# Kernel optimization log

Measured on AMD Instinct MI355X. Metric: run time of the kernel, lower is better.

Reference implementation:

```python
import jax, jax.numpy as jnp
import numpy as np

B, S, E = 4, 2048, 768
DFF = 4 * E
EPS = 1e-5


def _layernorm(x, g, b):
    mu = jnp.mean(x, axis=-1, keepdims=True)
    var = jnp.mean(jnp.square(x - mu), axis=-1, keepdims=True)
    return (x - mu) * jax.lax.rsqrt(var + EPS) * g + b


def setup_inputs() -> dict:
    key = jax.random.key(0)
    ks = jax.random.split(key, 16)
    w = lambda k, shp: jax.random.normal(k, shp, dtype=jnp.float32) * 0.02
    inp = {
        "x": jax.random.normal(ks[0], (B, S, E), dtype=jnp.float32),
        "kv": jax.random.normal(ks[1], (B, S, E), dtype=jnp.float32),
        "wq_w": w(ks[2], (E, E)), "wq_b": jnp.zeros((E,), jnp.float32),
        "wk_w": w(ks[3], (E, E)), "wk_b": jnp.zeros((E,), jnp.float32),
        "wv_w": w(ks[4], (E, E)), "wv_b": jnp.zeros((E,), jnp.float32),
        "ln1_g": jnp.ones((E,), jnp.float32), "ln1_b": jnp.zeros((E,), jnp.float32),
        "wq2_w": w(ks[5], (E, E)), "wq2_b": jnp.zeros((E,), jnp.float32),
        "wk2_w": w(ks[6], (E, E)), "wk2_b": jnp.zeros((E,), jnp.float32),
        "wv2_w": w(ks[7], (E, E)), "wv2_b": jnp.zeros((E,), jnp.float32),
        "ln2_g": jnp.ones((E,), jnp.float32), "ln2_b": jnp.zeros((E,), jnp.float32),
        "w1": w(ks[8], (DFF, E)), "b1": jnp.zeros((DFF,), jnp.float32),
        "w2": w(ks[9], (E, DFF)), "b2": jnp.zeros((E,), jnp.float32),
        "ln3_g": jnp.ones((E,), jnp.float32), "ln3_b": jnp.zeros((E,), jnp.float32),
    }
    return inp


def reference(x, kv, wq_w, wq_b, wk_w, wk_b, wv_w, wv_b, ln1_g, ln1_b,
              wq2_w, wq2_b, wk2_w, wk2_b, wv2_w, wv2_b, ln2_g, ln2_b,
              w1, b1, w2, b2, ln3_g, ln3_b):
    scalar = 1.0 / np.sqrt(E).astype(np.float32)
    mask_value = jnp.finfo(x.dtype).min
    s = x.shape[1]
    causal = jnp.triu(jnp.ones((s, s), dtype=bool), k=1)  # True above diagonal -> masked

    # ---- causal self-attention (single head, full E) ----
    q = x @ wq_w.T + wq_b
    k = x @ wk_w.T + wk_b
    v = x @ wv_w.T + wv_b
    scores = jnp.einsum('bqe,bke->bqk', q, k) * scalar
    scores = jnp.where(causal, mask_value, scores)
    h1 = jnp.einsum('bqk,bke->bqe', jax.nn.softmax(scores, axis=-1), v)
    x = _layernorm(x + h1, ln1_g, ln1_b)

    # ---- cross-attention over kv (no mask) ----
    q2 = x @ wq2_w.T + wq2_b
    k2 = kv @ wk2_w.T + wk2_b
    v2 = kv @ wv2_w.T + wv2_b
    scores2 = jnp.einsum('bqe,bke->bqk', q2, k2) * scalar
    h2 = jnp.einsum('bqk,bke->bqe', jax.nn.softmax(scores2, axis=-1), v2)
    x = _layernorm(x + h2, ln2_g, ln2_b)

    # ---- MLP: Linear -> ReLU -> Linear -> ReLU (note trailing ReLU) ----
    h = jax.nn.relu(x @ w1.T + b1)
    mlp = jax.nn.relu(h @ w2.T + b2)
    return _layernorm(x + mlp, ln3_g, ln3_b)
```

## Files before the change

### kernel.cpp

```cpp
#include <hip/hip_runtime.h>
#include <hip/hip_bf16.h>
#include <math.h>


typedef __bf16 bf16_t;
typedef bf16_t bf16x4 __attribute__((ext_vector_type(4)));
typedef bf16_t bf16x8 __attribute__((ext_vector_type(8)));
typedef float f32x4 __attribute__((ext_vector_type(4)));

struct MMDesc {
    const bf16_t* A;
    const bf16_t* B;
    const float* bias;
    __hip_bfloat16* C;
    float* lsum;
    int koff;
    int trans;
};
struct MMArgs { MMDesc g[8]; };

__device__ __forceinline__ int xcd_swz(int bid, int nwg) {
    const int q = nwg >> 3, r = nwg & 7;
    const int xcd = bid & 7, o = bid >> 3;
    const int base = (xcd < r) ? xcd * (q + 1) : r * (q + 1) + (xcd - r) * q;
    return base + o;
}

__device__ __forceinline__ void load16(const bf16_t* g, bf16_t* l) {
    __builtin_amdgcn_global_load_lds(
        (const __attribute__((address_space(1))) unsigned int*)g,
        (__attribute__((address_space(3))) unsigned int*)l, 16, 0, 0);
}

__device__ __forceinline__ void rd4(const bf16_t* p, int s0, int s1, bf16x8 f[4][2]) {
#pragma unroll
    for (int i = 0; i < 4; ++i) {
        f[i][0] = *(const bf16x8*)(p + i * 1024 + s0);
        f[i][1] = *(const bf16x8*)(p + i * 1024 + s1);
    }
}
__device__ __forceinline__ void rd2(const bf16_t* p, int s0, int s1, bf16x8 f[2][2]) {
#pragma unroll
    for (int i = 0; i < 2; ++i) {
        f[i][0] = *(const bf16x8*)(p + i * 1024 + s0);
        f[i][1] = *(const bf16x8*)(p + i * 1024 + s1);
    }
}

#define SBAR asm volatile("s_barrier" ::: "memory")
#define SCH  __builtin_amdgcn_sched_barrier(0)
#define PBAR do { SCH; SBAR; SCH; } while (0)
#define PRIO1 __builtin_amdgcn_s_setprio(1)
#define PRIO0 __builtin_amdgcn_s_setprio(0)
#define VMC6 asm volatile("s_waitcnt vmcnt(6)" ::: "memory")

#define QMFMA(mh, nh, BF) do { \
    _Pragma("unroll") \
    for (int ks = 0; ks < 2; ++ks) \
    _Pragma("unroll") \
    for (int mi = 0; mi < 4; ++mi) \
    _Pragma("unroll") \
    for (int ni = 0; ni < 2; ++ni) \
        acc[(mh) * 4 + mi][(nh) * 2 + ni] = __builtin_amdgcn_mfma_f32_16x16x32_bf16( \
            af[mi][ks], BF[ni][ks], acc[(mh) * 4 + mi][(nh) * 2 + ni], 0, 0, 0); \
} while (0)

__device__ __forceinline__ void mm8_core(
    const bf16_t* Ag, const bf16_t* Bg, int lda, int ldb, int K,
    bf16_t* lds, int w, int l, f32x4 acc[8][4])
{
    const long ldal = lda, ldbl = ldb;
    const int fr = l & 15, kq = l >> 4;
    const int rr = w * 8 + (l >> 3);
    const int c8e = ((l & 7) ^ (l >> 3)) * 8;
    const bf16_t* As = Ag + (long)rr * ldal + c8e;
    const bf16_t* Bs = Bg + (long)rr * ldbl + c8e;
    const int s0 = ((0 + kq) ^ (fr & 7)) * 8;
    const int s1 = ((4 + kq) ^ (fr & 7)) * 8;
    const bf16_t* lA = lds + ((w >> 2) * 64 + fr) * 64;
    const bf16_t* lB = lds + 16384 + ((w & 3) * 32 + fr) * 64;
    bf16_t* stA = lds + w * 512;
    bf16_t* stB = lds + 16384 + w * 512;

    auto stg = [&](int b, int isB, int h, int t) {
        const long ld = isB ? ldbl : ldal;
        const bf16_t* g = (isB ? Bs : As) + (long)h * 128 * ld + (long)t * 64;
        bf16_t* d = (isB ? stB : stA) + b * 32768 + h * 8192;
        load16(g, d);
        load16(g + 64 * ld, d + 4096);
    };

    bf16x8 af[4][2], bf0[2][2], bf1[2][2];
    const int NT = K >> 6, NI = NT >> 1;

    stg(0, 0, 0, 0); stg(0, 1, 0, 0); stg(0, 1, 1, 0); stg(0, 0, 1, 0);
    stg(1, 0, 0, 1); stg(1, 1, 0, 1); stg(1, 1, 1, 1);
    VMC6;
    SBAR; SCH;

    for (int i = 0; i < NI; ++i) {
        const int t1 = 2 * i + 1;
        int t2 = 2 * i + 2; if (t2 >= NT) t2 -= 2;
        int t3 = 2 * i + 3; if (t3 >= NT) t3 -= 2;
        rd4(lA, s0, s1, af); rd2(lB, s0, s1, bf0);
        stg(1, 0, 1, t1);
        PBAR; PRIO1; QMFMA(0, 0, bf0); PRIO0;
        rd2(lB + 8192, s0, s1, bf1);
        PBAR; PRIO1; QMFMA(0, 1, bf1); PRIO0;
        rd4(lA + 8192, s0, s1, af);
        stg(0, 0, 0, t2); stg(0, 1, 0, t2);
        PBAR; PRIO1; QMFMA(1, 0, bf0); PRIO0;
        stg(0, 1, 1, t2);
        VMC6;
        PBAR; PRIO1; QMFMA(1, 1, bf1); PRIO0;
        rd4(lA + 32768, s0, s1, af); rd2(lB + 32768, s0, s1, bf0);
        stg(0, 0, 1, t2);
        PBAR; PRIO1; QMFMA(0, 0, bf0); PRIO0;
        rd2(lB + 32768 + 8192, s0, s1, bf1);
        PBAR; PRIO1; QMFMA(0, 1, bf1); PRIO0;
        rd4(lA + 32768 + 8192, s0, s1, af);
        stg(1, 0, 0, t3); stg(1, 1, 0, t3);
        PBAR; PRIO1; QMFMA(1, 0, bf0); PRIO0;
        stg(1, 1, 1, t3);
        VMC6;
        PBAR; PRIO1; QMFMA(1, 1, bf1); PRIO0;
    }
    asm volatile("s_waitcnt vmcnt(0)" ::: "memory");
    SBAR; SCH;
}

template <bool RELU, bool CLAMPK>
__global__ __launch_bounds__(512, 2) void mm8_std(
    MMArgs args, int M, int N, int K, int lda, int ldb, float scale, int GX)
{
    __shared__ __align__(16) bf16_t lds[65536];
    const MMDesc dsc = args.g[blockIdx.z];

    const int lin = xcd_swz(blockIdx.x, gridDim.x);
    const int panel = lin / (8 * GX);
    const int rem = lin - panel * 8 * GX;
    const int bx = rem >> 3;
    const int by = panel * 8 + (rem & 7);
    const int m0 = by * 256, n0 = bx * 256;
    const int tid = threadIdx.x, w = tid >> 6, l = tid & 63;

    f32x4 acc[8][4];
    const f32x4 z4 = {0.f, 0.f, 0.f, 0.f};
#pragma unroll
    for (int i = 0; i < 8; ++i)
#pragma unroll
        for (int j = 0; j < 4; ++j) acc[i][j] = z4;

    int Keff = K;
    if (CLAMPK) {
        int km = (by + 1) * 256 - dsc.koff;
        Keff = km < K ? km : K;
    }
    if (!CLAMPK || Keff > 0)
        mm8_core(dsc.A + (long)m0 * lda, dsc.B + (long)n0 * ldb,
                 lda, ldb, Keff, lds, w, l, acc);

    const int fr = l & 15, erow = (l >> 4) * 4;
    const int wrow = (w >> 2) * 64, wcol = (w & 3) * 32;
    bf16_t* ctb = lds;
    __hip_bfloat16* ct = (__hip_bfloat16*)lds;
#pragma unroll
    for (int mh = 0; mh < 2; ++mh) {
        if (mh) __syncthreads();
#pragma unroll
        for (int nh = 0; nh < 2; ++nh)
#pragma unroll
            for (int ni = 0; ni < 2; ++ni) {
                const int cl = nh * 128 + wcol + ni * 16 + fr;
                const float bv = dsc.bias ? dsc.bias[n0 + cl] : 0.f;
#pragma unroll
                for (int mi = 0; mi < 4; ++mi) {
                    const int lr = wrow + mi * 16 + erow;
                    const f32x4 a = acc[mh * 4 + mi][nh * 2 + ni];
                    if (dsc.trans) {
                        bf16x4 p;
#pragma unroll
                        for (int r = 0; r < 4; ++r) {
                            float v = a[r] * scale + bv;
                            if (RELU) v = fmaxf(v, 0.f);
                            p[r] = (bf16_t)v;
                        }
                        *(bf16x4*)(ctb + cl * 140 + lr) = p;
                    } else {
#pragma unroll
                        for (int r = 0; r < 4; ++r) {
                            float v = a[r] * scale + bv;
                            if (RELU) v = fmaxf(v, 0.f);
                            ct[(lr + r) * 264 + cl] = __float2bfloat16(v);
                        }
                    }
                }
            }
        __syncthreads();
        if (dsc.trans) {
            __hip_bfloat16* base = dsc.C + ((long)(m0 >> 11) * N + n0) * 2048
                                 + (m0 & 2047) + mh * 128;
#pragma unroll
            for (int u = 0; u < 8; ++u) {
                const int e = u * 4096 + tid * 8;
                const int rl = e >> 7, cl = e & 127;
                const bf16_t* src = ctb + rl * 140 + cl;
                const uint2 lo = *(const uint2*)(src);
                const uint2 hi = *(const uint2*)(src + 4);
                const uint4 v = {lo.x, lo.y, hi.x, hi.y};
                *(uint4*)(base + (long)rl * 2048 + cl) = v;
            }
        } else {
            __hip_bfloat16* base = dsc.C + (long)(m0 + mh * 128) * N + n0;
#pragma unroll
            for (int u = 0; u < 8; ++u) {
                const int e = u * 4096 + tid * 8;
                *(uint4*)(base + (long)(e >> 8) * N + (e & 255))
                    = *(const uint4*)(ct + (e >> 8) * 264 + (e & 255));
            }
        }
    }
}

template <bool CAUSAL>
__global__ __launch_bounds__(512, 2) void mm8_exp(
    MMArgs args, int N, int K, int lda, int ldb, float scale, int GX)
{
    __shared__ __align__(16) bf16_t lds[65536];
    const MMDesc dsc = args.g[blockIdx.z];

    int bx, by;
    if (CAUSAL) {
        const int t = xcd_swz(blockIdx.x, gridDim.x);
        by = (int)((sqrtf(8.f * t + 1.f) - 1.f) * 0.5f);
        while ((by + 1) * (by + 2) / 2 <= t) ++by;
        while (by * (by + 1) / 2 > t) --by;
        bx = t - by * (by + 1) / 2;
    } else {
        const int lin = xcd_swz(blockIdx.x, gridDim.x);
        const int panel = lin / (8 * GX);
        const int rem = lin - panel * 8 * GX;
        bx = rem >> 3;
        by = panel * 8 + (rem & 7);
    }
    const int m0 = by * 256, n0 = bx * 256;
    const int tid = threadIdx.x, w = tid >> 6, l = tid & 63;

    f32x4 acc[8][4];
    const f32x4 z4 = {0.f, 0.f, 0.f, 0.f};
#pragma unroll
    for (int i = 0; i < 8; ++i)
#pragma unroll
        for (int j = 0; j < 4; ++j) acc[i][j] = z4;

    mm8_core(dsc.A + (long)m0 * lda, dsc.B + (long)n0 * ldb,
             lda, ldb, K, lds, w, l, acc);

    const int fr = l & 15, erow = (l >> 4) * 4;
    const int wrow = (w >> 2) * 64, wcol = (w & 3) * 32;
    __hip_bfloat16* ct = (__hip_bfloat16*)lds;
#pragma unroll
    for (int mh = 0; mh < 2; ++mh) {
        if (mh) __syncthreads();
#pragma unroll
        for (int mi = 0; mi < 4; ++mi) {
            const int lr = wrow + mi * 16 + erow;
#pragma unroll
            for (int r = 0; r < 4; ++r) {
                const int grow = m0 + mh * 128 + lr + r;
                float rs = 0.f;
#pragma unroll
                for (int nh = 0; nh < 2; ++nh)
#pragma unroll
                    for (int ni = 0; ni < 2; ++ni) {
                        const int cl = nh * 128 + wcol + ni * 16 + fr;
                        float e;
                        if (CAUSAL && (n0 + cl) > grow)
                            e = 0.f;
                        else
                            e = __expf(acc[mh * 4 + mi][nh * 2 + ni][r] * scale);
                        ct[(lr + r) * 264 + cl] = __float2bfloat16(e);
                        rs += e;
                    }
#pragma unroll
                for (int o = 8; o > 0; o >>= 1) rs += __shfl_down(rs, o, 16);
                if ((l & 15) == 0) atomicAdd(&dsc.lsum[grow], rs);
            }
        }
        __syncthreads();
        __hip_bfloat16* base = dsc.C + (long)(m0 + mh * 128) * N + n0;
#pragma unroll
        for (int u = 0; u < 8; ++u) {
            const int e = u * 4096 + tid * 8;
            *(uint4*)(base + (long)(e >> 8) * N + (e & 255))
                = *(const uint4*)(ct + (e >> 8) * 264 + (e & 255));
        }
    }
}

__device__ __forceinline__ float waveReduceSum(float v) {
#pragma unroll
    for (int o = 32; o > 0; o >>= 1) v += __shfl_down(v, o, 64);
    return v;
}
__device__ __forceinline__ float blockReduceSum(float v, float* s) {
    int lane = threadIdx.x & 63, w = threadIdx.x >> 6;
    v = waveReduceSum(v);
    __syncthreads();
    if (lane == 0) s[w] = v;
    __syncthreads();
    return s[0] + s[1] + s[2] + s[3];
}

template <bool BR, bool XF32>
__global__ __launch_bounds__(256) void ln_kernel(
    const float* __restrict__ xf, const __hip_bfloat16* __restrict__ xh,
    const __hip_bfloat16* __restrict__ h1, const __hip_bfloat16* __restrict__ h2,
    const float* __restrict__ hbias, const float* __restrict__ lsum,
    const float* __restrict__ g, const float* __restrict__ beta,
    float* __restrict__ outf, __hip_bfloat16* __restrict__ outb) {
    __shared__ float red[4];
    const int E = 768;
    const long row = blockIdx.x;
    const float hscale = lsum ? (1.f / lsum[row]) : 1.f;

    float vals[3];
    float sum = 0.f;
#pragma unroll
    for (int i = 0; i < 3; ++i) {
        int c = threadIdx.x + i * 256;
        float t = __bfloat162float(h1[row * E + c]) + __bfloat162float(h2[row * E + c]);
        if (BR) t = fmaxf(t + hbias[c], 0.f);
        else t *= hscale;
        float xv = XF32 ? xf[row * E + c] : __bfloat162float(xh[row * E + c]);
        vals[i] = xv + t;
        sum += vals[i];
    }
    sum = blockReduceSum(sum, red);
    const float mean = sum * (1.f / 768.f);

    float ss = 0.f;
#pragma unroll
    for (int i = 0; i < 3; ++i) {
        float d = vals[i] - mean;
        ss += d * d;
    }
    ss = blockReduceSum(ss, red);
    const float inv = rsqrtf(ss * (1.f / 768.f) + 1e-5f);

#pragma unroll
    for (int i = 0; i < 3; ++i) {
        int c = threadIdx.x + i * 256;
        float v = (vals[i] - mean) * inv * g[c] + beta[c];
        if (outf) outf[row * E + c] = v;
        if (outb) outb[row * E + c] = __float2bfloat16(v);
    }
}

struct CvtPtrs {
    const float* s[10];
    __hip_bfloat16* d[10];
};
__global__ __launch_bounds__(256) void cvt_all(CvtPtrs p) {
    int bid = blockIdx.x, seg, off;
    if (bid < 3456) {
        seg = bid / 576;
        off = (bid % 576) * 1024;
    } else if (bid < 8064) {
        int t = bid - 3456;
        seg = 6 + t / 2304;
        off = (t % 2304) * 1024;
    } else {
        int t = bid - 8064;
        seg = 8 + t / 6144;
        off = (t % 6144) * 1024;
    }
    const float* s = p.s[seg];
    __hip_bfloat16* d = p.d[seg];
    int i = off + threadIdx.x * 4;
    float4 v = *(const float4*)(s + i);
    d[i + 0] = __float2bfloat16(v.x);
    d[i + 1] = __float2bfloat16(v.y);
    d[i + 2] = __float2bfloat16(v.z);
    d[i + 3] = __float2bfloat16(v.w);
}

extern "C" void kernel_launch(void* const* d_in, const int* in_sizes, int n_in,
                              void* d_out, int out_size, void* d_ws, size_t ws_size,
                              hipStream_t stream) {
    const int Bb = 4, S = 2048, E = 768, DFF = 3072;
    const int Nr = Bb * S;

    const float* x    = (const float*)d_in[0];
    const float* kv   = (const float*)d_in[1];
    const float* wq_w = (const float*)d_in[2];
    const float* wq_b = (const float*)d_in[3];
    const float* wk_w = (const float*)d_in[4];
    const float* wk_b = (const float*)d_in[5];
    const float* wv_w = (const float*)d_in[6];
    const float* wv_b = (const float*)d_in[7];
    const float* ln1g = (const float*)d_in[8];
    const float* ln1b = (const float*)d_in[9];
    const float* wq2w = (const float*)d_in[10];
    const float* wq2b = (const float*)d_in[11];
    const float* wk2w = (const float*)d_in[12];
    const float* wk2b = (const float*)d_in[13];
    const float* wv2w = (const float*)d_in[14];
    const float* wv2b = (const float*)d_in[15];
    const float* ln2g = (const float*)d_in[16];
    const float* ln2b = (const float*)d_in[17];
    const float* w1   = (const float*)d_in[18];
    const float* b1   = (const float*)d_in[19];
    const float* w2   = (const float*)d_in[20];
    const float* b2   = (const float*)d_in[21];
    const float* ln3g = (const float*)d_in[22];
    const float* ln3b = (const float*)d_in[23];
    float* out = (float*)d_out;

    char* wsp = (char*)d_ws;
    auto alloc = [&](size_t bytes) {
        char* p = wsp;
        wsp += (bytes + 255) & ~(size_t)255;
        return p;
    };
    const size_t nSE = (size_t)Nr * E;
    const size_t nSS = (size_t)Bb * S * S;
    __hip_bfloat16* Pb   = (__hip_bfloat16*)alloc(nSS * 2);
    __hip_bfloat16* qb   = (__hip_bfloat16*)alloc(nSE * 2);
    __hip_bfloat16* kb   = (__hip_bfloat16*)alloc(nSE * 2);
    __hip_bfloat16* hffb = Pb;
    __hip_bfloat16* vtb  = (__hip_bfloat16*)alloc(nSE * 2);
    __hip_bfloat16* xb   = (__hip_bfloat16*)alloc(nSE * 2);
    __hip_bfloat16* kvb  = (__hip_bfloat16*)alloc(nSE * 2);
    __hip_bfloat16* actb = (__hip_bfloat16*)alloc(nSE * 2);
    __hip_bfloat16* hA   = (__hip_bfloat16*)alloc(nSE * 2);
    __hip_bfloat16* hB   = (__hip_bfloat16*)alloc(nSE * 2);
    __hip_bfloat16* wqb   = (__hip_bfloat16*)alloc((size_t)E * E * 2);
    __hip_bfloat16* wkb   = (__hip_bfloat16*)alloc((size_t)E * E * 2);
    __hip_bfloat16* wvb   = (__hip_bfloat16*)alloc((size_t)E * E * 2);
    __hip_bfloat16* wq2bm = (__hip_bfloat16*)alloc((size_t)E * E * 2);
    __hip_bfloat16* wk2bm = (__hip_bfloat16*)alloc((size_t)E * E * 2);
    __hip_bfloat16* wv2bm = (__hip_bfloat16*)alloc((size_t)E * E * 2);
    __hip_bfloat16* w1b   = (__hip_bfloat16*)alloc((size_t)DFF * E * 2);
    __hip_bfloat16* w2b   = (__hip_bfloat16*)alloc((size_t)E * DFF * 2);
    float* lsum1 = (float*)alloc((size_t)Nr * 4);
    float* lsum2 = (float*)alloc((size_t)Nr * 4);

    __hip_bfloat16* k2b  = (__hip_bfloat16*)d_out;
    __hip_bfloat16* vtb2 = k2b + nSE;

    const float scale = 1.0f / sqrtf((float)E);
    const dim3 blk(256);
    const dim3 blk5(512);

    hipMemsetAsync(lsum1, 0, (size_t)Nr * 4 * 2, stream);

    CvtPtrs cp;
    cp.s[0] = wq_w; cp.d[0] = wqb;
    cp.s[1] = wk_w; cp.d[1] = wkb;
    cp.s[2] = wv_w; cp.d[2] = wvb;
    cp.s[3] = wq2w; cp.d[3] = wq2bm;
    cp.s[4] = wk2w; cp.d[4] = wk2bm;
    cp.s[5] = wv2w; cp.d[5] = wv2bm;
    cp.s[6] = w1;   cp.d[6] = w1b;
    cp.s[7] = w2;   cp.d[7] = w2b;
    cp.s[8] = x;    cp.d[8] = xb;
    cp.s[9] = kv;   cp.d[9] = kvb;
    cvt_all<<<8064 + 12288, blk, 0, stream>>>(cp);

    {
        MMArgs a{};
        a.g[0] = {(const bf16_t*)xb,  (const bf16_t*)wqb,   wq_b, qb,   nullptr, 0, 0};
        a.g[1] = {(const bf16_t*)xb,  (const bf16_t*)wkb,   wk_b, kb,   nullptr, 0, 0};
        a.g[2] = {(const bf16_t*)xb,  (const bf16_t*)wvb,   wv_b, vtb,  nullptr, 0, 1};
        a.g[3] = {(const bf16_t*)kvb, (const bf16_t*)wk2bm, wk2b, k2b,  nullptr, 0, 0};
        a.g[4] = {(const bf16_t*)kvb, (const bf16_t*)wv2bm, wv2b, vtb2, nullptr, 0, 1};
        mm8_std<false, false><<<dim3(96, 1, 5), blk5, 0, stream>>>(
            a, Nr, E, E, E, E, 1.f, 3);
    }
    {
        MMArgs a{};
        for (int b = 0; b < 4; ++b)
            a.g[b] = {(const bf16_t*)qb + (long)b * S * E,
                      (const bf16_t*)kb + (long)b * S * E, nullptr,
                      Pb + (long)b * S * S, lsum1 + b * S, 0, 0};
        mm8_exp<true><<<dim3(36, 1, 4), blk5, 0, stream>>>(a, S, E, E, E, scale, 8);
    }
    {
        MMArgs a{};
        for (int b = 0; b < 4; ++b)
            for (int ks = 0; ks < 2; ++ks)
                a.g[b * 2 + ks] = {(const bf16_t*)Pb + (long)b * S * S + ks * 1024,
                                   (const bf16_t*)vtb + (long)b * E * S + ks * 1024,
                                   nullptr, (ks ? hB : hA) + (long)b * S * E,
                                   nullptr, ks * 1024, 0};
        mm8_std<false, true><<<dim3(24, 1, 8), blk5, 0, stream>>>(
            a, S, E, 1024, S, S, 1.f, 3);
    }
    ln_kernel<false, true><<<Nr, blk, 0, stream>>>(
        x, nullptr, hA, hB, nullptr, lsum1, ln1g, ln1b, nullptr, actb);

    {
        MMArgs a{};
        a.g[0] = {(const bf16_t*)actb, (const bf16_t*)wq2bm, wq2b, qb, nullptr, 0, 0};
        mm8_std<false, false><<<dim3(96, 1, 1), blk5, 0, stream>>>(
            a, Nr, E, E, E, E, 1.f, 3);
    }
    {
        MMArgs a{};
        for (int b = 0; b < 4; ++b)
            a.g[b] = {(const bf16_t*)qb + (long)b * S * E,
                      (const bf16_t*)k2b + (long)b * S * E, nullptr,
                      Pb + (long)b * S * S, lsum2 + b * S, 0, 0};
        mm8_exp<false><<<dim3(64, 1, 4), blk5, 0, stream>>>(a, S, E, E, E, scale, 8);
    }
    {
        MMArgs a{};
        for (int b = 0; b < 4; ++b)
            for (int ks = 0; ks < 2; ++ks)
                a.g[b * 2 + ks] = {(const bf16_t*)Pb + (long)b * S * S + ks * 1024,
                                   (const bf16_t*)vtb2 + (long)b * E * S + ks * 1024,
                                   nullptr, (ks ? hB : hA) + (long)b * S * E,
                                   nullptr, 0, 0};
        mm8_std<false, false><<<dim3(24, 1, 8), blk5, 0, stream>>>(
            a, S, E, 1024, S, S, 1.f, 3);
    }
    ln_kernel<false, false><<<Nr, blk, 0, stream>>>(
        nullptr, actb, hA, hB, nullptr, lsum2, ln2g, ln2b, nullptr, actb);

    {
        MMArgs a{};
        a.g[0] = {(const bf16_t*)actb, (const bf16_t*)w1b, b1, hffb, nullptr, 0, 0};
        mm8_std<true, false><<<dim3(384, 1, 1), blk5, 0, stream>>>(
            a, Nr, DFF, E, E, E, 1.f, 12);
    }
    {
        MMArgs a{};
        a.g[0] = {(const bf16_t*)hffb, (const bf16_t*)w2b, nullptr, hA, nullptr, 0, 0};
        a.g[1] = {(const bf16_t*)hffb + 1536, (const bf16_t*)w2b + 1536, nullptr,
                  hB, nullptr, 0, 0};
        mm8_std<false, false><<<dim3(96, 1, 2), blk5, 0, stream>>>(
            a, Nr, E, 1536, DFF, DFF, 1.f, 3);
    }
    ln_kernel<true, false><<<Nr, blk, 0, stream>>>(
        nullptr, actb, hA, hB, b2, nullptr, ln3g, ln3b, out, nullptr);
}
```

Baseline: 496.8 us.

## Precompute LDS read pointers, add partial lgkm wait, fold memset into convert kernel

The GEMM core now precomputes per-half LDS read pointers and global staging pointers, which reduces address arithmetic in the hot loop. It also inserts an s_waitcnt lgkmcnt(8) before the first MFMA group of each half-iteration. The separate hipMemsetAsync that zeroed the softmax row sums is folded into the conversion kernel as 16 extra blocks, removing one launch. The first layernorm now reads the bf16 copy of x instead of fp32 x, which cuts bandwidth but loses residual precision.

```diff
diff --git a/kernel.cpp b/kernel.cpp
--- a/kernel.cpp
+++ b/kernel.cpp
@@ -32,18 +32,20 @@
         (__attribute__((address_space(3))) unsigned int*)l, 16, 0, 0);
 }
 
-__device__ __forceinline__ void rd4(const bf16_t* p, int s0, int s1, bf16x8 f[4][2]) {
+__device__ __forceinline__ void rd4h(const bf16_t* p0, const bf16_t* p1, int H,
+                                     bf16x8 f[4][2]) {
 #pragma unroll
     for (int i = 0; i < 4; ++i) {
-        f[i][0] = *(const bf16x8*)(p + i * 1024 + s0);
-        f[i][1] = *(const bf16x8*)(p + i * 1024 + s1);
-    }
-}
-__device__ __forceinline__ void rd2(const bf16_t* p, int s0, int s1, bf16x8 f[2][2]) {
+        f[i][0] = *(const bf16x8*)(p0 + H + i * 1024);
+        f[i][1] = *(const bf16x8*)(p1 + H + i * 1024);
+    }
+}
+__device__ __forceinline__ void rd2h(const bf16_t* p0, const bf16_t* p1, int H,
+                                     bf16x8 f[2][2]) {
 #pragma unroll
     for (int i = 0; i < 2; ++i) {
-        f[i][0] = *(const bf16x8*)(p + i * 1024 + s0);
-        f[i][1] = *(const bf16x8*)(p + i * 1024 + s1);
+        f[i][0] = *(const bf16x8*)(p0 + H + i * 1024);
+        f[i][1] = *(const bf16x8*)(p1 + H + i * 1024);
     }
 }
 
@@ -53,6 +55,7 @@
 #define PRIO1 __builtin_amdgcn_s_setprio(1)
 #define PRIO0 __builtin_amdgcn_s_setprio(0)
 #define VMC6 asm volatile("s_waitcnt vmcnt(6)" ::: "memory")
+#define LGK8 do { asm volatile("s_waitcnt lgkmcnt(8)" ::: "memory"); } while (0)
 
 #define QMFMA(mh, nh, BF) do { \
     _Pragma("unroll") \
@@ -73,21 +76,32 @@
     const int fr = l & 15, kq = l >> 4;
     const int rr = w * 8 + (l >> 3);
     const int c8e = ((l & 7) ^ (l >> 3)) * 8;
-    const bf16_t* As = Ag + (long)rr * ldal + c8e;
-    const bf16_t* Bs = Bg + (long)rr * ldbl + c8e;
+    const bf16_t* pA[2];
+    const bf16_t* pB[2];
+    pA[0] = Ag + (long)rr * ldal + c8e;
+    pA[1] = pA[0] + 128 * ldal;
+    pB[0] = Bg + (long)rr * ldbl + c8e;
+    pB[1] = pB[0] + 128 * ldbl;
     const int s0 = ((0 + kq) ^ (fr & 7)) * 8;
     const int s1 = ((4 + kq) ^ (fr & 7)) * 8;
-    const bf16_t* lA = lds + ((w >> 2) * 64 + fr) * 64;
-    const bf16_t* lB = lds + 16384 + ((w & 3) * 32 + fr) * 64;
+    const int arow = ((w >> 2) * 64 + fr) * 64;
+    const int brow = ((w & 3) * 32 + fr) * 64;
+    const bf16_t* lA0s0 = lds + arow + s0;
+    const bf16_t* lA0s1 = lds + arow + s1;
+    const bf16_t* lA1s0 = lds + 32768 + arow + s0;
+    const bf16_t* lA1s1 = lds + 32768 + arow + s1;
+    const bf16_t* lB0s0 = lds + 16384 + brow + s0;
+    const bf16_t* lB0s1 = lds + 16384 + brow + s1;
+    const bf16_t* lB1s0 = lds + 49152 + brow + s0;
+    const bf16_t* lB1s1 = lds + 49152 + brow + s1;
     bf16_t* stA = lds + w * 512;
     bf16_t* stB = lds + 16384 + w * 512;
 
     auto stg = [&](int b, int isB, int h, int t) {
-        const long ld = isB ? ldbl : ldal;
-        const bf16_t* g = (isB ? Bs : As) + (long)h * 128 * ld + (long)t * 64;
+        const bf16_t* g = (isB ? pB[h] : pA[h]) + (long)t * 64;
         bf16_t* d = (isB ? stB : stA) + b * 32768 + h * 8192;
         load16(g, d);
-        load16(g + 64 * ld, d + 4096);
+        load16(g + 64 * (isB ? ldbl : ldal), d + 4096);
     };
 
     bf16x8 af[4][2], bf0[2][2], bf1[2][2];
@@ -102,23 +116,25 @@
         const int t1 = 2 * i + 1;
         int t2 = 2 * i + 2; if (t2 >= NT) t2 -= 2;
         int t3 = 2 * i + 3; if (t3 >= NT) t3 -= 2;
-        rd4(lA, s0, s1, af); rd2(lB, s0, s1, bf0);
+        rd4h(lA0s0, lA0s1, 0, af); rd2h(lB0s0, lB0s1, 0, bf0);
         stg(1, 0, 1, t1);
+        LGK8;
         PBAR; PRIO1; QMFMA(0, 0, bf0); PRIO0;
-        rd2(lB + 8192, s0, s1, bf1);
+        rd2h(lB0s0, lB0s1, 8192, bf1);
         PBAR; PRIO1; QMFMA(0, 1, bf1); PRIO0;
-        rd4(lA + 8192, s0, s1, af);
+        rd4h(lA0s0, lA0s1, 8192, af);
         stg(0, 0, 0, t2); stg(0, 1, 0, t2);
         PBAR; PRIO1; QMFMA(1, 0, bf0); PRIO0;
         stg(0, 1, 1, t2);
         VMC6;
         PBAR; PRIO1; QMFMA(1, 1, bf1); PRIO0;
-        rd4(lA + 32768, s0, s1, af); rd2(lB + 32768, s0, s1, bf0);
+        rd4h(lA1s0, lA1s1, 0, af); rd2h(lB1s0, lB1s1, 0, bf0);
         stg(0, 0, 1, t2);
+        LGK8;
         PBAR; PRIO1; QMFMA(0, 0, bf0); PRIO0;
-        rd2(lB + 32768 + 8192, s0, s1, bf1);
+        rd2h(lB1s0, lB1s1, 8192, bf1);
         PBAR; PRIO1; QMFMA(0, 1, bf1); PRIO0;
-        rd4(lA + 32768 + 8192, s0, s1, af);
+        rd4h(lA1s0, lA1s1, 8192, af);
         stg(1, 0, 0, t3); stg(1, 1, 0, t3);
         PBAR; PRIO1; QMFMA(1, 0, bf0); PRIO0;
         stg(1, 1, 1, t3);
@@ -360,9 +376,16 @@
 struct CvtPtrs {
     const float* s[10];
     __hip_bfloat16* d[10];
+    float* zero;
 };
 __global__ __launch_bounds__(256) void cvt_all(CvtPtrs p) {
     int bid = blockIdx.x, seg, off;
+    if (bid >= 20352) {
+        int i = (bid - 20352) * 1024 + threadIdx.x * 4;
+        float4 z = {0.f, 0.f, 0.f, 0.f};
+        *(float4*)(p.zero + i) = z;
+        return;
+    }
     if (bid < 3456) {
         seg = bid / 576;
         off = (bid % 576) * 1024;
@@ -453,8 +476,6 @@
     const dim3 blk(256);
     const dim3 blk5(512);
 
-    hipMemsetAsync(lsum1, 0, (size_t)Nr * 4 * 2, stream);
-
     CvtPtrs cp;
     cp.s[0] = wq_w; cp.d[0] = wqb;
     cp.s[1] = wk_w; cp.d[1] = wkb;
@@ -466,7 +487,8 @@
     cp.s[7] = w2;   cp.d[7] = w2b;
     cp.s[8] = x;    cp.d[8] = xb;
     cp.s[9] = kv;   cp.d[9] = kvb;
-    cvt_all<<<8064 + 12288, blk, 0, stream>>>(cp);
+    cp.zero = lsum1;
+    cvt_all<<<8064 + 12288 + 16, blk, 0, stream>>>(cp);
 
     {
         MMArgs a{};
@@ -497,8 +519,8 @@
         mm8_std<false, true><<<dim3(24, 1, 8), blk5, 0, stream>>>(
             a, S, E, 1024, S, S, 1.f, 3);
     }
-    ln_kernel<false, true><<<Nr, blk, 0, stream>>>(
-        x, nullptr, hA, hB, nullptr, lsum1, ln1g, ln1b, nullptr, actb);
+    ln_kernel<false, false><<<Nr, blk, 0, stream>>>(
+        nullptr, xb, hA, hB, nullptr, lsum1, ln1g, ln1b, nullptr, actb);
 
     {
         MMArgs a{};
```

After: 502.0 us. About the same (+1.0%).
